# Kernel optimization log

Measured on AMD Instinct MI355X. Metric: run time of the kernel, lower is better.

The kernel has to match this reference:

```python
import jax, jax.numpy as jnp
import numpy as np

BANDWIDTH = 1.0


def setup_inputs() -> dict:
    key = jax.random.key(0)
    k1, k2 = jax.random.split(key)
    test_Xs = jax.random.normal(k1, (4096, 16), dtype=jnp.float32)
    train_Xs = jax.random.normal(k2, (8192, 16), dtype=jnp.float32)
    return {"test_Xs": test_Xs, "train_Xs": train_Xs}


def reference(test_Xs, train_Xs):
    n, d = train_Xs.shape
    h = jnp.float32(BANDWIDTH)
    # log normalization constant of n Gaussian kernels with bandwidth h in d dims
    Z = 0.5 * d * jnp.log(2 * jnp.float32(np.pi)) + d * jnp.log(h) + jnp.log(jnp.float32(n))
    # diffs: [n_test, n_train, d]
    diffs = (test_Xs[:, None, :] - train_Xs[None, :, :]) / h
    log_exp = -0.5 * jnp.sum(diffs * diffs, axis=-1)  # [n_test, n_train]
    return jax.scipy.special.logsumexp(log_exp - Z, axis=-1)  # [n_test]
```

## Files before the change

### kernel.cpp

```cpp
#include <hip/hip_runtime.h>
#include <math.h>

#define LOG2E 1.4426950408889634f
#define LN2   0.6931471805599453f
#define NW 16
#define CH 64

typedef short short8 __attribute__((ext_vector_type(8)));
typedef float f32x16 __attribute__((ext_vector_type(16)));

__device__ inline unsigned int cvtpk_bf16(float lo, float hi) {
    unsigned int r;
    asm("v_cvt_pk_bf16_f32 %0, %1, %2" : "=v"(r) : "v"(lo), "v"(hi));
    return r;
}

__global__ __launch_bounds__(1024, 4) void kde_fused(
    const float* __restrict__ testX, const float* __restrict__ trainX,
    float* __restrict__ out, int nTest, int nTrain, int nch, float Z)
{
    const int tid  = threadIdx.x;
    const int lane = tid & 63;
    const int w    = tid >> 6;
    const int c    = lane & 31;
    const int half = lane >> 5;
    const int rowBase = blockIdx.x * 32;

    __shared__ short8 stage[NW][2 * CH];
    __shared__ float  wbuf[NW][CH];
    __shared__ float  xnbuf[32];
    __shared__ __align__(16) float red2[NW][32][36];
    __shared__ float  red3[32][33];

    const int mrow = min(rowBase + c, nTest - 1);
    const float4* xp = (const float4*)(testX + (size_t)mrow * 16) + half * 2;
    float4 xa = xp[0], xb = xp[1];
    float f0 = xa.x*LOG2E, f1 = xa.y*LOG2E, f2 = xa.z*LOG2E, f3 = xa.w*LOG2E;
    float f4 = xb.x*LOG2E, f5 = xb.y*LOG2E, f6 = xb.z*LOG2E, f7 = xb.w*LOG2E;
    float pn = ((f0*f0 + f1*f1) + (f2*f2 + f3*f3))
             + ((f4*f4 + f5*f5) + (f6*f6 + f7*f7));
    float xn2 = (pn + __shfl_xor(pn, 32)) * (0.5f / LOG2E);
    union { unsigned int u[4]; short8 s; } au;
    au.u[0] = cvtpk_bf16(f0, f1);
    au.u[1] = cvtpk_bf16(f2, f3);
    au.u[2] = cvtpk_bf16(f4, f5);
    au.u[3] = cvtpk_bf16(f6, f7);
    const short8 afrag = au.s;
    if (w == 0 && half == 0) xnbuf[c] = xn2;

    const int nMax = nTrain - 1;
    const int tb   = w * nch * CH;
    const int rdU  = (c * 2 + half) ^ ((c >> 2) & 7);

    float4 q0, q1, q2, q3; float wv;
    auto LOADRAW = [&](int ch) {
        int gi = tb + ch * CH + lane;
        const float4* p = (const float4*)(trainX + (size_t)min(gi, nMax) * 16);
        q0 = p[0]; q1 = p[1]; q2 = p[2]; q3 = p[3];
        float nrm = ((q0.x*q0.x + q0.y*q0.y) + (q0.z*q0.z + q0.w*q0.w))
                  + ((q1.x*q1.x + q1.y*q1.y) + (q1.z*q1.z + q1.w*q1.w))
                  + ((q2.x*q2.x + q2.y*q2.y) + (q2.z*q2.z + q2.w*q2.w))
                  + ((q3.x*q3.x + q3.y*q3.y) + (q3.z*q3.z + q3.w*q3.w));
        wv = (gi <= nMax) ? __builtin_amdgcn_exp2f(-0.5f * LOG2E * nrm) : 0.0f;
    };
    auto WRITEPT = [&]() {
        const int pp = lane & 31, ti = lane >> 5;
        const int u0 = (pp * 2 + 0) ^ ((pp >> 2) & 7);
        const int u1 = (pp * 2 + 1) ^ ((pp >> 2) & 7);
        union { unsigned int u[4]; short8 s; } b0, b1;
        b0.u[0] = cvtpk_bf16(q0.x, q0.y); b0.u[1] = cvtpk_bf16(q0.z, q0.w);
        b0.u[2] = cvtpk_bf16(q1.x, q1.y); b0.u[3] = cvtpk_bf16(q1.z, q1.w);
        b1.u[0] = cvtpk_bf16(q2.x, q2.y); b1.u[1] = cvtpk_bf16(q2.z, q2.w);
        b1.u[2] = cvtpk_bf16(q3.x, q3.y); b1.u[3] = cvtpk_bf16(q3.z, q3.w);
        stage[w][ti * 64 + u0] = b0.s;
        stage[w][ti * 64 + u1] = b1.s;
        wbuf[w][lane] = wv;
    };

    float rs[16];
    #pragma unroll
    for (int i = 0; i < 16; ++i) rs[i] = 0.0f;

    auto INNER = [&]() {
        #pragma unroll
        for (int t = 0; t < 2; ++t) {
            short8 bf = stage[w][t * 64 + rdU];
            float  wt = wbuf[w][t * 32 + c];
            f32x16 z = {0.f,0.f,0.f,0.f,0.f,0.f,0.f,0.f,
                        0.f,0.f,0.f,0.f,0.f,0.f,0.f,0.f};
            f32x16 d = __builtin_amdgcn_mfma_f32_32x32x16_bf16(afrag, bf, z, 0,0,0);
            #pragma unroll
            for (int r = 0; r < 16; ++r)
                rs[r] += __builtin_amdgcn_exp2f(d[r]) * wt;
        }
    };

    LOADRAW(0);
    WRITEPT();
    for (int ch = 0; ch < nch - 1; ++ch) {
        LOADRAW(ch + 1);
        INNER();
        WRITEPT();
    }
    INNER();

    #pragma unroll
    for (int qd = 0; qd < 4; ++qd) {
        float4 v = make_float4(rs[qd*4+0], rs[qd*4+1], rs[qd*4+2], rs[qd*4+3]);
        *(float4*)&red2[w][c][half * 4 + qd * 8] = v;
    }
    __syncthreads();

    {
        int row = tid & 31, seg = tid >> 5;
        int wv2 = seg >> 1, cb = (seg & 1) * 16;
        float s = 0.0f;
        #pragma unroll
        for (int i = 0; i < 16; ++i) s += red2[wv2][cb + i][row];
        red3[row][seg] = s;
    }
    __syncthreads();

    if (tid < 32) {
        int row = rowBase + tid;
        if (row < nTest) {
            float s = 0.0f;
            #pragma unroll
            for (int k = 0; k < 32; ++k) s += red3[tid][k];
            out[row] = __logf(s) - xnbuf[tid] * LN2 - Z;
        }
    }
}

extern "C" void kernel_launch(void* const* d_in, const int* in_sizes, int n_in,
                              void* d_out, int out_size, void* d_ws, size_t ws_size,
                              hipStream_t stream) {
    const float* testX  = (const float*)d_in[0];
    const float* trainX = (const float*)d_in[1];
    float* out = (float*)d_out;

    const int D = 16;
    const int nTest  = in_sizes[0] / D;
    const int nTrain = in_sizes[1] / D;

    const float Z = 0.5f * (float)D * logf(2.0f * (float)M_PI) + logf((float)nTrain);

    const int nch  = (nTrain + NW * CH - 1) / (NW * CH);
    const int grid = (nTest + 31) / 32;

    kde_fused<<<grid, 1024, 0, stream>>>(testX, trainX, out, nTest, nTrain, nch, Z);
}
```

Measured before the change: 16.15 us.

## Halve test rows per block to double grid size across CUs

Each block now handles 16 test rows instead of 32. The A fragment duplicates the 16 rows into both halves of the 32x32 MFMA tile, and only the 8 accumulator entries for unique rows are exponentiated. Reduction buffers and the grid size are adjusted to match, so twice as many blocks run and more of the device's compute units have work. In exchange, each block still loads and converts the full training set, so that redundant global traffic doubles and half of each MFMA's output is discarded.

```diff
diff --git a/kernel.cpp b/kernel.cpp
--- a/kernel.cpp
+++ b/kernel.cpp
@@ -24,15 +24,15 @@
     const int w    = tid >> 6;
     const int c    = lane & 31;
     const int half = lane >> 5;
-    const int rowBase = blockIdx.x * 32;
+    const int rowBase = blockIdx.x * 16;
 
     __shared__ short8 stage[NW][2 * CH];
     __shared__ float  wbuf[NW][CH];
-    __shared__ float  xnbuf[32];
-    __shared__ __align__(16) float red2[NW][32][36];
-    __shared__ float  red3[32][33];
+    __shared__ float  xnbuf[16];
+    __shared__ __align__(16) float red2[NW][32][20];
+    __shared__ float  red3[16][68];
 
-    const int mrow = min(rowBase + c, nTest - 1);
+    const int mrow = min(rowBase + (c & 15), nTest - 1);
     const float4* xp = (const float4*)(testX + (size_t)mrow * 16) + half * 2;
     float4 xa = xp[0], xb = xp[1];
     float f0 = xa.x*LOG2E, f1 = xa.y*LOG2E, f2 = xa.z*LOG2E, f3 = xa.w*LOG2E;
@@ -46,7 +46,7 @@
     au.u[2] = cvtpk_bf16(f4, f5);
     au.u[3] = cvtpk_bf16(f6, f7);
     const short8 afrag = au.s;
-    if (w == 0 && half == 0) xnbuf[c] = xn2;
+    if (w == 0 && half == 0 && c < 16) xnbuf[c] = xn2;
 
     const int nMax = nTrain - 1;
     const int tb   = w * nch * CH;
@@ -77,22 +77,25 @@
         wbuf[w][lane] = wv;
     };
 
-    float rs[16];
+    float rs[8];
     #pragma unroll
-    for (int i = 0; i < 16; ++i) rs[i] = 0.0f;
+    for (int i = 0; i < 8; ++i) rs[i] = 0.0f;
 
+    const f32x16 zc = {0.f,0.f,0.f,0.f,0.f,0.f,0.f,0.f,
+                       0.f,0.f,0.f,0.f,0.f,0.f,0.f,0.f};
     auto INNER = [&]() {
+        short8 bf0 = stage[w][rdU];
+        short8 bf1 = stage[w][64 + rdU];
+        float  wt0 = wbuf[w][c];
+        float  wt1 = wbuf[w][32 + c];
+        f32x16 d0 = __builtin_amdgcn_mfma_f32_32x32x16_bf16(afrag, bf0, zc, 0,0,0);
+        f32x16 d1 = __builtin_amdgcn_mfma_f32_32x32x16_bf16(afrag, bf1, zc, 0,0,0);
         #pragma unroll
-        for (int t = 0; t < 2; ++t) {
-            short8 bf = stage[w][t * 64 + rdU];
-            float  wt = wbuf[w][t * 32 + c];
-            f32x16 z = {0.f,0.f,0.f,0.f,0.f,0.f,0.f,0.f,
-                        0.f,0.f,0.f,0.f,0.f,0.f,0.f,0.f};
-            f32x16 d = __builtin_amdgcn_mfma_f32_32x32x16_bf16(afrag, bf, z, 0,0,0);
-            #pragma unroll
-            for (int r = 0; r < 16; ++r)
-                rs[r] += __builtin_amdgcn_exp2f(d[r]) * wt;
-        }
+        for (int r = 0; r < 8; ++r)
+            rs[r] += __builtin_amdgcn_exp2f(d0[r]) * wt0;
+        #pragma unroll
+        for (int r = 0; r < 8; ++r)
+            rs[r] += __builtin_amdgcn_exp2f(d1[r]) * wt1;
     };
 
     LOADRAW(0);
@@ -104,29 +107,30 @@
     }
     INNER();
 
-    #pragma unroll
-    for (int qd = 0; qd < 4; ++qd) {
-        float4 v = make_float4(rs[qd*4+0], rs[qd*4+1], rs[qd*4+2], rs[qd*4+3]);
-        *(float4*)&red2[w][c][half * 4 + qd * 8] = v;
+    {
+        float4 v0 = make_float4(rs[0], rs[1], rs[2], rs[3]);
+        float4 v1 = make_float4(rs[4], rs[5], rs[6], rs[7]);
+        *(float4*)&red2[w][c][half * 4]     = v0;
+        *(float4*)&red2[w][c][8 + half * 4] = v1;
     }
     __syncthreads();
 
     {
-        int row = tid & 31, seg = tid >> 5;
-        int wv2 = seg >> 1, cb = (seg & 1) * 16;
+        int row = tid & 15, seg = tid >> 4;
+        int wv2 = seg >> 2, cb = (seg & 3) * 8;
         float s = 0.0f;
         #pragma unroll
-        for (int i = 0; i < 16; ++i) s += red2[wv2][cb + i][row];
+        for (int i = 0; i < 8; ++i) s += red2[wv2][cb + i][row];
         red3[row][seg] = s;
     }
     __syncthreads();
 
-    if (tid < 32) {
+    if (tid < 16) {
         int row = rowBase + tid;
         if (row < nTest) {
             float s = 0.0f;
             #pragma unroll
-            for (int k = 0; k < 32; ++k) s += red3[tid][k];
+            for (int k = 0; k < 64; ++k) s += red3[tid][k];
             out[row] = __logf(s) - xnbuf[tid] * LN2 - Z;
         }
     }
@@ -146,7 +150,7 @@
     const float Z = 0.5f * (float)D * logf(2.0f * (float)M_PI) + logf((float)nTrain);
 
     const int nch  = (nTrain + NW * CH - 1) / (NW * CH);
-    const int grid = (nTest + 31) / 32;
+    const int grid = (nTest + 15) / 16;
 
     kde_fused<<<grid, 1024, 0, stream>>>(testX, trainX, out, nTest, nTrain, nch, Z);
 }
```

New measurement: 14.95 us, median of 2. 7.5% less time.
